# Performance work log

Hardware: AMD Instinct MI355X
Metric: run time of the kernel (lower is better)

The kernel has to match this reference:

```python
import jax, jax.numpy as jnp
import numpy as np

L, D, H, F = 4, 1024, 16, 4096  # layers, d_model, heads, ffn hidden
DH = D // H
B, S = 2, 1024


def layer_norm(x, g, b, eps=1e-12):
    m = jnp.mean(x, axis=-1, keepdims=True)
    v = jnp.mean((x - m) ** 2, axis=-1, keepdims=True)
    return (x - m) / jnp.sqrt(v + eps) * g + b


def setup_inputs() -> dict:
    key = jax.random.key(0)
    ks = jax.random.split(key, 8)
    std = 0.02
    inp = {
        'x': jax.random.normal(ks[0], (B, S, D), dtype=jnp.float32),
        'attn_mask': jnp.ones((B, S), dtype=jnp.int32),
        'Wq': jax.random.normal(ks[1], (L, D, D), dtype=jnp.float32) * std,
        'bq': jnp.zeros((L, D), dtype=jnp.float32),
        'Wk': jax.random.normal(ks[2], (L, D, D), dtype=jnp.float32) * std,
        'bk': jnp.zeros((L, D), dtype=jnp.float32),
        'Wv': jax.random.normal(ks[3], (L, D, D), dtype=jnp.float32) * std,
        'bv': jnp.zeros((L, D), dtype=jnp.float32),
        'Wo': jax.random.normal(ks[4], (L, D, D), dtype=jnp.float32) * std,
        'bo': jnp.zeros((L, D), dtype=jnp.float32),
        'ln1_g': jnp.ones((L, D), dtype=jnp.float32),
        'ln1_b': jnp.zeros((L, D), dtype=jnp.float32),
        'W1': jax.random.normal(ks[5], (L, D, F), dtype=jnp.float32) * std,
        'b1': jnp.zeros((L, F), dtype=jnp.float32),
        'W2': jax.random.normal(ks[6], (L, F, D), dtype=jnp.float32) * std,
        'b2': jnp.zeros((L, D), dtype=jnp.float32),
        'ln2_g': jnp.ones((L, D), dtype=jnp.float32),
        'ln2_b': jnp.zeros((L, D), dtype=jnp.float32),
    }
    return inp


def _block(h, mask, Wq, bq, Wk, bk, Wv, bv, Wo, bo, ln1_g, ln1_b, W1, b1, W2, b2, ln2_g, ln2_b):
    b, s, _ = h.shape
    def heads(t):
        return t.reshape(b, s, H, DH).transpose(0, 2, 1, 3)  # (b, h, s, dh)
    q = heads(jnp.einsum('bsd,de->bse', h, Wq) + bq) / jnp.sqrt(jnp.float32(DH))
    k = heads(jnp.einsum('bsd,de->bse', h, Wk) + bk)
    v = heads(jnp.einsum('bsd,de->bse', h, Wv) + bv)
    scores = jnp.einsum('bhqd,bhkd->bhqk', q, k)
    scores = jnp.where(mask[:, None, None, :] == 0, -jnp.inf, scores)
    w = jax.nn.softmax(scores, axis=-1)
    ctx = jnp.einsum('bhqk,bhkd->bhqd', w, v)
    ctx = ctx.transpose(0, 2, 1, 3).reshape(b, s, D)
    sa = jnp.einsum('bsd,de->bse', ctx, Wo) + bo
    h = layer_norm(sa + h, ln1_g, ln1_b)
    ff = jnp.einsum('bsd,df->bsf', h, W1) + b1
    ff = jax.nn.gelu(ff, approximate=False)
    ff = jnp.einsum('bsf,fd->bsd', ff, W2) + b2
    return layer_norm(ff + h, ln2_g, ln2_b)


def reference(x, attn_mask, Wq, bq, Wk, bk, Wv, bv, Wo, bo, ln1_g, ln1_b, W1, b1, W2, b2, ln2_g, ln2_b):
    h = x
    for i in range(L):
        h = _block(h, attn_mask, Wq[i], bq[i], Wk[i], bk[i], Wv[i], bv[i], Wo[i], bo[i],
                   ln1_g[i], ln1_b[i], W1[i], b1[i], W2[i], b2[i], ln2_g[i], ln2_b[i])
    return h
```

## Files before the change

kernel.cpp:

```cpp
#include <hip/hip_runtime.h>
#include <cstdint>
#include <cstddef>

using bf16x8 = __attribute__((ext_vector_type(8))) short;
using f32x4  = __attribute__((ext_vector_type(4))) float;

__device__ __forceinline__ unsigned short f2bf(float f) {
  unsigned int u = __builtin_bit_cast(unsigned int, f);
  u += 0x7fffu + ((u >> 16) & 1u);
  return (unsigned short)(u >> 16);
}
__device__ __forceinline__ float bf2f(unsigned short h) {
  unsigned int u = ((unsigned int)h) << 16;
  return __builtin_bit_cast(float, u);
}

__device__ __forceinline__ void async_cp16(const void* g, void* l) {
  __builtin_amdgcn_global_load_lds(
      (__attribute__((address_space(1))) void*)(g),
      (__attribute__((address_space(3))) void*)(l), 16, 0, 0);
}

struct EpParams {
  const float* bias;
  const float* bias2;
  const float* bias3;
  const float* res;
  float* outf;
  unsigned short* outb;
  unsigned short* outb2;
  unsigned short* outb3;
  long long strideCz;
  int ldC;
  int pair_base;
};

template <int BM, int BN, int WGM, int WGN, int FI, int FJ, int EP>
__global__ __launch_bounds__(256, 2) void gemm_bt(
    const unsigned short* __restrict__ A, const unsigned short* __restrict__ B,
    int K, int kTiles, long long strideAz, long long strideBz, EpParams p) {
  __shared__ alignas(16) unsigned short As[BM * 64];
  __shared__ alignas(16) unsigned short Bs[BN * 64];
  const int t = threadIdx.x;
  const int lane = t & 63;
  const int w = t >> 6;
  const int wr = w / WGN, wc = w % WGN;
  const int lm = lane & 15, quad = lane >> 4;
  const int m0 = blockIdx.y * BM, n0 = blockIdx.x * BN;
  const int bz = blockIdx.z;
  A += (long long)bz * strideAz;
  B += (long long)bz * strideBz;

  f32x4 acc[FI][FJ] = {};

  const int rowA = t >> 3;
  const int colSw = ((t & 7) ^ (rowA & 7)) * 8;

  for (int kt = 0; kt < kTiles; ++kt) {
    const unsigned short* ga = A + (size_t)(m0 + rowA) * K + kt * 64 + colSw;
    const unsigned short* gb = B + (size_t)(n0 + rowA) * K + kt * 64 + colSw;
#pragma unroll
    for (int s = 0; s < BM / 32; ++s)
      async_cp16(ga + (size_t)s * 32 * K, &As[s * 2048 + t * 8]);
#pragma unroll
    for (int s = 0; s < BN / 32; ++s)
      async_cp16(gb + (size_t)s * 32 * K, &Bs[s * 2048 + t * 8]);
    __syncthreads();
#pragma unroll
    for (int ks = 0; ks < 2; ++ks) {
      bf16x8 af[FI], bfr[FJ];
#pragma unroll
      for (int i = 0; i < FI; ++i) {
        int ra = wr * FI * 16 + i * 16 + lm;
        af[i] = *(const bf16x8*)&As[ra * 64 + (((ks * 4 + quad) ^ (ra & 7)) << 3)];
      }
#pragma unroll
      for (int j = 0; j < FJ; ++j) {
        int rb = wc * FJ * 16 + j * 16 + lm;
        bfr[j] = *(const bf16x8*)&Bs[rb * 64 + (((ks * 4 + quad) ^ (rb & 7)) << 3)];
      }
#pragma unroll
      for (int i = 0; i < FI; ++i)
#pragma unroll
        for (int j = 0; j < FJ; ++j)
          acc[i][j] = __builtin_amdgcn_mfma_f32_16x16x32_bf16(af[i], bfr[j], acc[i][j], 0, 0, 0);
    }
    __syncthreads();
  }

#pragma unroll
  for (int i = 0; i < FI; ++i) {
#pragma unroll
    for (int j = 0; j < FJ; ++j) {
#pragma unroll
      for (int r = 0; r < 4; ++r) {
        int row = m0 + wr * FI * 16 + i * 16 + quad * 4 + r;
        int col = n0 + wc * FJ * 16 + j * 16 + lm;
        float v = acc[i][j][r];
        if constexpr (EP == 1) {
          p.outb[(long long)bz * p.strideCz + ((size_t)row << 10) + col] = f2bf(v);
        } else if constexpr (EP == 0) {
          int bb = row >> 10, s = row & 1023;
          if (col < 1024) {
            float q = (v + p.bias[col]) * 0.125f;
            int hd = col >> 6, dh = col & 63;
            p.outb[((size_t)(bb * 16 + hd) << 16) + (s << 6) + dh] = f2bf(q);
          } else if (col < 2048) {
            int c2 = col - 1024;
            float kk = v + p.bias2[c2];
            int hd = c2 >> 6, dh = c2 & 63;
            p.outb2[((size_t)(bb * 16 + hd) << 16) + (s << 6) + dh] = f2bf(kk);
          } else {
            int c3 = col - 2048;
            float vv = v + p.bias3[c3];
            int hd = c3 >> 6, dh = c3 & 63;
            p.outb3[((size_t)(bb * 16 + hd) << 16) + ((size_t)dh << 10) + s] = f2bf(vv);
          }
        } else if constexpr (EP == 2) {
          int pair = p.pair_base + bz;
          int bb = pair >> 4, hd = pair & 15;
          p.outb[((size_t)bb << 20) + ((size_t)row << 10) + (hd << 6) + col] = f2bf(v);
        } else if constexpr (EP == 3) {
          size_t idx = (size_t)row * p.ldC + col;
          float add = (bz == 0) ? (p.bias[col] + p.res[idx]) : 0.0f;
          p.outf[(long long)bz * p.strideCz + idx] = v + add;
        } else if constexpr (EP == 4) {
          float val = v + p.bias[col];
          float g = 0.5f * val * (1.0f + erff(val * 0.70710678118654752f));
          p.outb[(size_t)row * p.ldC + col] = f2bf(g);
        }
      }
    }
  }
}

__global__ __launch_bounds__(256) void transpose_w(
    const float* __restrict__ Wq, const float* __restrict__ Wk,
    const float* __restrict__ Wv, const float* __restrict__ Wo,
    const float* __restrict__ W1, const float* __restrict__ W2,
    unsigned short* __restrict__ wqkv, unsigned short* __restrict__ wo,
    unsigned short* __restrict__ w1, unsigned short* __restrict__ w2) {
  int blk = blockIdx.x;
  int kind, local;
  if (blk < 1024) { kind = blk >> 8; local = blk & 255; }
  else if (blk < 2048) { kind = 4; local = blk - 1024; }
  else { kind = 5; local = blk - 2048; }
  const float* src;
  unsigned short* dst;
  int K, N;
  switch (kind) {
    case 0: src = Wq; dst = wqkv;                  K = 1024; N = 1024; break;
    case 1: src = Wk; dst = wqkv + 1024 * 1024;    K = 1024; N = 1024; break;
    case 2: src = Wv; dst = wqkv + 2048 * 1024;    K = 1024; N = 1024; break;
    case 3: src = Wo; dst = wo;                    K = 1024; N = 1024; break;
    case 4: src = W1; dst = w1;                    K = 1024; N = 4096; break;
    default: src = W2; dst = w2;                   K = 4096; N = 1024; break;
  }
  int tilesK = K >> 6;
  int tk = local % tilesK, tn = local / tilesK;
  int k0 = tk << 6, n0 = tn << 6;
  __shared__ float lds[64][65];
  int t = threadIdx.x;
  int rr = t >> 4, cc = (t & 15) * 4;
#pragma unroll
  for (int pp = 0; pp < 4; ++pp) {
    float4 v = *(const float4*)&src[(size_t)(k0 + rr + pp * 16) * N + n0 + cc];
    lds[rr + pp * 16][cc + 0] = v.x;
    lds[rr + pp * 16][cc + 1] = v.y;
    lds[rr + pp * 16][cc + 2] = v.z;
    lds[rr + pp * 16][cc + 3] = v.w;
  }
  __syncthreads();
#pragma unroll
  for (int pp = 0; pp < 4; ++pp) {
    int nr = rr + pp * 16;
    ushort4 o;
    o.x = f2bf(lds[cc + 0][nr]);
    o.y = f2bf(lds[cc + 1][nr]);
    o.z = f2bf(lds[cc + 2][nr]);
    o.w = f2bf(lds[cc + 3][nr]);
    *(ushort4*)&dst[(size_t)(n0 + nr) * K + k0 + cc] = o;
  }
}

__global__ __launch_bounds__(256) void cvt_bf16(const float* __restrict__ in,
                                                unsigned short* __restrict__ out) {
  int i = (blockIdx.x * 256 + threadIdx.x) * 4;
  float4 v = *(const float4*)&in[i];
  ushort4 o;
  o.x = f2bf(v.x); o.y = f2bf(v.y); o.z = f2bf(v.z); o.w = f2bf(v.w);
  *(ushort4*)&out[i] = o;
}

__global__ __launch_bounds__(256) void softmax_k(unsigned short* __restrict__ Sc,
                                                 const int* __restrict__ mask) {
  int rowid = blockIdx.x;
  int pair = rowid >> 10;
  int q = rowid & 1023;
  int bb = pair >> 4;
  unsigned short* srow = Sc + ((size_t)pair << 20) + ((size_t)q << 10);
  const int* mrow = mask + (bb << 10);
  int t = threadIdx.x;
  ushort4 s4 = *(const ushort4*)&srow[t * 4];
  int4 m4 = *(const int4*)&mrow[t * 4];
  float v0 = m4.x ? bf2f(s4.x) : -1e30f;
  float v1 = m4.y ? bf2f(s4.y) : -1e30f;
  float v2 = m4.z ? bf2f(s4.z) : -1e30f;
  float v3 = m4.w ? bf2f(s4.w) : -1e30f;
  float mx = fmaxf(fmaxf(v0, v1), fmaxf(v2, v3));
  for (int o = 32; o > 0; o >>= 1) mx = fmaxf(mx, __shfl_xor(mx, o));
  __shared__ float red[4];
  __shared__ float red2[4];
  if ((t & 63) == 0) red[t >> 6] = mx;
  __syncthreads();
  mx = fmaxf(fmaxf(red[0], red[1]), fmaxf(red[2], red[3]));
  float e0 = (v0 > -1e29f) ? __expf(v0 - mx) : 0.f;
  float e1 = (v1 > -1e29f) ? __expf(v1 - mx) : 0.f;
  float e2 = (v2 > -1e29f) ? __expf(v2 - mx) : 0.f;
  float e3 = (v3 > -1e29f) ? __expf(v3 - mx) : 0.f;
  float sum = e0 + e1 + e2 + e3;
  for (int o = 32; o > 0; o >>= 1) sum += __shfl_xor(sum, o);
  if ((t & 63) == 0) red2[t >> 6] = sum;
  __syncthreads();
  sum = red2[0] + red2[1] + red2[2] + red2[3];
  float inv = 1.0f / sum;
  ushort4 o4;
  o4.x = f2bf(e0 * inv); o4.y = f2bf(e1 * inv);
  o4.z = f2bf(e2 * inv); o4.w = f2bf(e3 * inv);
  *(ushort4*)&srow[t * 4] = o4;
}

__global__ __launch_bounds__(256) void ln_k(const float* __restrict__ in,
                                            const float* __restrict__ in2,
                                            const float* __restrict__ g,
                                            const float* __restrict__ b,
                                            float* __restrict__ outf,
                                            unsigned short* __restrict__ outb) {
  int row = blockIdx.x;
  int t = threadIdx.x;
  const float* x = in + ((size_t)row << 10);
  const float* x2 = in2 + ((size_t)row << 10);
  float4 v = *(const float4*)&x[t * 4];
  float4 v2 = *(const float4*)&x2[t * 4];
  v.x += v2.x; v.y += v2.y; v.z += v2.z; v.w += v2.w;
  float s1 = v.x + v.y + v.z + v.w;
  float s2 = v.x * v.x + v.y * v.y + v.z * v.z + v.w * v.w;
  for (int o = 32; o > 0; o >>= 1) {
    s1 += __shfl_xor(s1, o);
    s2 += __shfl_xor(s2, o);
  }
  __shared__ float r1[4], r2[4];
  if ((t & 63) == 0) { r1[t >> 6] = s1; r2[t >> 6] = s2; }
  __syncthreads();
  s1 = r1[0] + r1[1] + r1[2] + r1[3];
  s2 = r2[0] + r2[1] + r2[2] + r2[3];
  float mean = s1 * (1.0f / 1024.0f);
  float var = s2 * (1.0f / 1024.0f) - mean * mean;
  float rstd = rsqrtf(var + 1e-12f);
  float4 gg = *(const float4*)&g[t * 4];
  float4 bb = *(const float4*)&b[t * 4];
  float o0 = (v.x - mean) * rstd * gg.x + bb.x;
  float o1 = (v.y - mean) * rstd * gg.y + bb.y;
  float o2 = (v.z - mean) * rstd * gg.z + bb.z;
  float o3 = (v.w - mean) * rstd * gg.w + bb.w;
  float4 of = make_float4(o0, o1, o2, o3);
  *(float4*)&outf[((size_t)row << 10) + t * 4] = of;
  ushort4 ob;
  ob.x = f2bf(o0); ob.y = f2bf(o1); ob.z = f2bf(o2); ob.w = f2bf(o3);
  *(ushort4*)&outb[((size_t)row << 10) + t * 4] = ob;
}

extern "C" void kernel_launch(void* const* d_in, const int* in_sizes, int n_in,
                              void* d_out, int out_size, void* d_ws, size_t ws_size,
                              hipStream_t stream) {
  (void)in_sizes; (void)n_in; (void)out_size; (void)ws_size;
  const float* x    = (const float*)d_in[0];
  const int*   mask = (const int*)d_in[1];
  const float* Wq   = (const float*)d_in[2];
  const float* bq   = (const float*)d_in[3];
  const float* Wk   = (const float*)d_in[4];
  const float* bk   = (const float*)d_in[5];
  const float* Wv   = (const float*)d_in[6];
  const float* bv   = (const float*)d_in[7];
  const float* Wo   = (const float*)d_in[8];
  const float* bo   = (const float*)d_in[9];
  const float* ln1g = (const float*)d_in[10];
  const float* ln1b = (const float*)d_in[11];
  const float* W1   = (const float*)d_in[12];
  const float* b1   = (const float*)d_in[13];
  const float* W2   = (const float*)d_in[14];
  const float* b2   = (const float*)d_in[15];
  const float* ln2g = (const float*)d_in[16];
  const float* ln2b = (const float*)d_in[17];
  float* out = (float*)d_out;

  char* wsp = (char*)d_ws;
  auto take = [&](size_t bytes) { char* r = wsp; wsp += bytes; return r; };
  unsigned short* wqkv = (unsigned short*)take(3072ull * 1024 * 2);
  unsigned short* wo_t = (unsigned short*)take(1024ull * 1024 * 2);
  unsigned short* w1_t = (unsigned short*)take(4096ull * 1024 * 2);
  unsigned short* w2_t = (unsigned short*)take(1024ull * 4096 * 2);
  float*          h    = (float*)take(2048ull * 1024 * 4);
  unsigned short* hbf  = (unsigned short*)take(2048ull * 1024 * 2);
  unsigned short* Qb   = (unsigned short*)take(2048ull * 1024 * 2);
  unsigned short* Kbuf = (unsigned short*)take(2048ull * 1024 * 2);
  unsigned short* VTb  = (unsigned short*)take(2048ull * 1024 * 2);
  unsigned short* ctxb = (unsigned short*)take(2048ull * 1024 * 2);
  float*          tmp  = (float*)take(2ull * 2048 * 1024 * 4);
  unsigned short* scr  = (unsigned short*)take(32ull * 1024 * 1024 * 2);
  unsigned short* ffb  = scr;
  const long long TMPZ = 2048ll * 1024;

  cvt_bf16<<<2048, 256, 0, stream>>>(x, hbf);

  for (int l = 0; l < 4; ++l) {
    transpose_w<<<3072, 256, 0, stream>>>(
        Wq + (size_t)l * 1048576, Wk + (size_t)l * 1048576,
        Wv + (size_t)l * 1048576, Wo + (size_t)l * 1048576,
        W1 + (size_t)l * 4194304, W2 + (size_t)l * 4194304,
        wqkv, wo_t, w1_t, w2_t);

    {
      EpParams p{};
      p.bias = bq + l * 1024; p.bias2 = bk + l * 1024; p.bias3 = bv + l * 1024;
      p.outb = Qb; p.outb2 = Kbuf; p.outb3 = VTb;
      gemm_bt<64, 128, 2, 2, 2, 4, 0><<<dim3(24, 32, 1), 256, 0, stream>>>(
          hbf, wqkv, 1024, 16, 0, 0, p);
    }

    {
      EpParams p{};
      p.outb = scr; p.strideCz = 1 << 20;
      gemm_bt<128, 128, 2, 2, 4, 4, 1><<<dim3(8, 8, 32), 256, 0, stream>>>(
          Qb, Kbuf, 64, 1, 65536, 65536, p);
    }
    softmax_k<<<32768, 256, 0, stream>>>(scr, mask);
    {
      EpParams p{};
      p.outb = ctxb; p.pair_base = 0;
      gemm_bt<64, 64, 2, 2, 2, 2, 2><<<dim3(1, 16, 32), 256, 0, stream>>>(
          scr, VTb, 1024, 16, 1 << 20, 65536, p);
    }

    {
      EpParams p{};
      p.bias = bo + l * 1024; p.res = (l == 0 ? x : h);
      p.outf = tmp; p.strideCz = TMPZ; p.ldC = 1024;
      gemm_bt<128, 64, 2, 2, 4, 2, 3><<<dim3(16, 16, 2), 256, 0, stream>>>(
          ctxb, wo_t, 1024, 8, 512, 512, p);
    }
    ln_k<<<2048, 256, 0, stream>>>(tmp, tmp + TMPZ,
                                   ln1g + l * 1024, ln1b + l * 1024, h, hbf);

    {
      EpParams p{};
      p.bias = b1 + l * 4096; p.outb = ffb; p.ldC = 4096;
      gemm_bt<64, 128, 2, 2, 2, 4, 4><<<dim3(32, 32, 1), 256, 0, stream>>>(
          hbf, w1_t, 1024, 16, 0, 0, p);
    }
    {
      EpParams p{};
      p.bias = b2 + l * 1024; p.res = h;
      p.outf = tmp; p.strideCz = TMPZ; p.ldC = 1024;
      gemm_bt<128, 64, 2, 2, 4, 2, 3><<<dim3(16, 16, 2), 256, 0, stream>>>(
          ffb, w2_t, 4096, 32, 2048, 2048, p);
    }
    ln_k<<<2048, 256, 0, stream>>>(tmp, tmp + TMPZ,
                                   ln2g + l * 1024, ln2b + l * 1024,
                                   (l == 3 ? out : h), hbf);
  }
}
```

Baseline: 1.015 ms.

## Fuse QK^T, softmax and PV into a single flash-attention kernel

Replaces the three-kernel attention path (score GEMM writing a 32x1024x1024 bf16 score matrix, a separate softmax pass, then the PV GEMM) with one flash-attention kernel that uses online softmax over 128-key tiles held in LDS. This removes the large score-matrix round trips through global memory and two kernel launches per layer. In exchange the kernel launches only 512 blocks with serialized per-tile work, which may limit occupancy, and the probabilities are rounded to bf16 before PV as before.

```diff
diff --git a/kernel.cpp b/kernel.cpp
--- a/kernel.cpp
+++ b/kernel.cpp
@@ -97,9 +97,7 @@
         int row = m0 + wr * FI * 16 + i * 16 + quad * 4 + r;
         int col = n0 + wc * FJ * 16 + j * 16 + lm;
         float v = acc[i][j][r];
-        if constexpr (EP == 1) {
-          p.outb[(long long)bz * p.strideCz + ((size_t)row << 10) + col] = f2bf(v);
-        } else if constexpr (EP == 0) {
+        if constexpr (EP == 0) {
           int bb = row >> 10, s = row & 1023;
           if (col < 1024) {
             float q = (v + p.bias[col]) * 0.125f;
@@ -116,10 +114,6 @@
             int hd = c3 >> 6, dh = c3 & 63;
             p.outb3[((size_t)(bb * 16 + hd) << 16) + ((size_t)dh << 10) + s] = f2bf(vv);
           }
-        } else if constexpr (EP == 2) {
-          int pair = p.pair_base + bz;
-          int bb = pair >> 4, hd = pair & 15;
-          p.outb[((size_t)bb << 20) + ((size_t)row << 10) + (hd << 6) + col] = f2bf(v);
         } else if constexpr (EP == 3) {
           size_t idx = (size_t)row * p.ldC + col;
           float add = (bz == 0) ? (p.bias[col] + p.res[idx]) : 0.0f;
@@ -131,6 +125,162 @@
         }
       }
     }
+  }
+}
+
+__global__ __launch_bounds__(256, 2) void flash_attn(
+    const unsigned short* __restrict__ Qb, const unsigned short* __restrict__ Kb,
+    const unsigned short* __restrict__ VTb, const int* __restrict__ mask,
+    unsigned short* __restrict__ ctx) {
+  __shared__ alignas(16) unsigned short Qs[64 * 64];
+  __shared__ alignas(16) unsigned short Ks[128 * 64];
+  __shared__ alignas(16) unsigned short VTs[64 * 128];
+  __shared__ alignas(16) unsigned short Ps[64 * 128];
+  const int t = threadIdx.x;
+  const int lane = t & 63;
+  const int w = t >> 6;
+  const int lm = lane & 15, quad = lane >> 4;
+  const int pair = blockIdx.y;
+  const int q0 = blockIdx.x * 64;
+  const int bb = pair >> 4, hd = pair & 15;
+  const unsigned short* Qp = Qb + ((size_t)pair << 16);
+  const unsigned short* Kp = Kb + ((size_t)pair << 16);
+  const unsigned short* Vp = VTb + ((size_t)pair << 16);
+  const int* mrow = mask + (bb << 10);
+
+  {
+    const int rowA = t >> 3;
+    const int c = t & 7;
+#pragma unroll
+    for (int s = 0; s < 2; ++s) {
+      int row = s * 32 + rowA;
+      async_cp16(Qp + (size_t)(q0 + row) * 64 + ((c ^ (row & 7)) << 3),
+                 &Qs[s * 2048 + t * 8]);
+    }
+  }
+
+  f32x4 o_acc[4] = {};
+  float m_run[4], l_run[4];
+#pragma unroll
+  for (int r = 0; r < 4; ++r) { m_run[r] = -3e38f; l_run[r] = 0.f; }
+
+  for (int k0 = 0; k0 < 1024; k0 += 128) {
+    __syncthreads();
+    {
+      const int rowA = t >> 3;
+      const int c = t & 7;
+#pragma unroll
+      for (int s = 0; s < 4; ++s) {
+        int row = s * 32 + rowA;
+        async_cp16(Kp + (size_t)(k0 + row) * 64 + ((c ^ (row & 7)) << 3),
+                   &Ks[s * 2048 + t * 8]);
+      }
+      const int rowV = t >> 4;
+      const int cv = t & 15;
+#pragma unroll
+      for (int s = 0; s < 4; ++s) {
+        int row = s * 16 + rowV;
+        async_cp16(Vp + (size_t)row * 1024 + k0 + ((cv ^ (row & 15)) << 3),
+                   &VTs[s * 2048 + t * 8]);
+      }
+    }
+    int mv[8];
+#pragma unroll
+    for (int j = 0; j < 8; ++j) mv[j] = mrow[k0 + j * 16 + lm];
+    __syncthreads();
+
+    f32x4 s_acc[8] = {};
+    {
+      const int ra = w * 16 + lm;
+      bf16x8 aq[2];
+#pragma unroll
+      for (int ks = 0; ks < 2; ++ks)
+        aq[ks] = *(const bf16x8*)&Qs[ra * 64 + (((ks * 4 + quad) ^ (ra & 7)) << 3)];
+#pragma unroll
+      for (int j = 0; j < 8; ++j) {
+        const int rb = j * 16 + lm;
+#pragma unroll
+        for (int ks = 0; ks < 2; ++ks) {
+          bf16x8 bk_ = *(const bf16x8*)&Ks[rb * 64 + (((ks * 4 + quad) ^ (rb & 7)) << 3)];
+          s_acc[j] = __builtin_amdgcn_mfma_f32_16x16x32_bf16(aq[ks], bk_, s_acc[j], 0, 0, 0);
+        }
+      }
+    }
+
+    float mt[4];
+#pragma unroll
+    for (int r = 0; r < 4; ++r) mt[r] = -3e38f;
+#pragma unroll
+    for (int j = 0; j < 8; ++j)
+#pragma unroll
+      for (int r = 0; r < 4; ++r) {
+        float sv = mv[j] ? s_acc[j][r] : -1e30f;
+        s_acc[j][r] = sv;
+        mt[r] = fmaxf(mt[r], sv);
+      }
+#pragma unroll
+    for (int r = 0; r < 4; ++r)
+#pragma unroll
+      for (int off = 1; off < 16; off <<= 1)
+        mt[r] = fmaxf(mt[r], __shfl_xor(mt[r], off));
+    float alpha[4], lt[4];
+#pragma unroll
+    for (int r = 0; r < 4; ++r) {
+      float mn = fmaxf(m_run[r], mt[r]);
+      alpha[r] = __expf(m_run[r] - mn);
+      m_run[r] = mn;
+      lt[r] = 0.f;
+    }
+#pragma unroll
+    for (int j = 0; j < 8; ++j)
+#pragma unroll
+      for (int r = 0; r < 4; ++r) {
+        float pv = __expf(s_acc[j][r] - m_run[r]);
+        s_acc[j][r] = pv;
+        lt[r] += pv;
+      }
+#pragma unroll
+    for (int r = 0; r < 4; ++r) {
+#pragma unroll
+      for (int off = 1; off < 16; off <<= 1) lt[r] += __shfl_xor(lt[r], off);
+      l_run[r] = l_run[r] * alpha[r] + lt[r];
+    }
+#pragma unroll
+    for (int jf = 0; jf < 4; ++jf)
+#pragma unroll
+      for (int r = 0; r < 4; ++r) o_acc[jf][r] *= alpha[r];
+
+#pragma unroll
+    for (int j = 0; j < 8; ++j) {
+      const int chunk = 2 * j + (lm >> 3);
+#pragma unroll
+      for (int r = 0; r < 4; ++r) {
+        const int row = w * 16 + quad * 4 + r;
+        Ps[row * 128 + ((chunk ^ (row & 15)) << 3) + (lm & 7)] = f2bf(s_acc[j][r]);
+      }
+    }
+
+    const int ra = w * 16 + lm;
+#pragma unroll
+    for (int kk = 0; kk < 4; ++kk) {
+      bf16x8 ap = *(const bf16x8*)&Ps[ra * 128 + (((kk * 4 + quad) ^ (ra & 15)) << 3)];
+#pragma unroll
+      for (int jf = 0; jf < 4; ++jf) {
+        const int rb = jf * 16 + lm;
+        bf16x8 bv_ = *(const bf16x8*)&VTs[rb * 128 + (((kk * 4 + quad) ^ (rb & 15)) << 3)];
+        o_acc[jf] = __builtin_amdgcn_mfma_f32_16x16x32_bf16(ap, bv_, o_acc[jf], 0, 0, 0);
+      }
+    }
+  }
+
+#pragma unroll
+  for (int r = 0; r < 4; ++r) {
+    float inv = 1.0f / l_run[r];
+    int row = q0 + w * 16 + quad * 4 + r;
+#pragma unroll
+    for (int jf = 0; jf < 4; ++jf)
+      ctx[((size_t)bb << 20) + ((size_t)row << 10) + (hd << 6) + jf * 16 + lm] =
+          f2bf(o_acc[jf][r] * inv);
   }
 }
 
@@ -190,44 +340,6 @@
   ushort4 o;
   o.x = f2bf(v.x); o.y = f2bf(v.y); o.z = f2bf(v.z); o.w = f2bf(v.w);
   *(ushort4*)&out[i] = o;
-}
-
-__global__ __launch_bounds__(256) void softmax_k(unsigned short* __restrict__ Sc,
-                                                 const int* __restrict__ mask) {
-  int rowid = blockIdx.x;
-  int pair = rowid >> 10;
-  int q = rowid & 1023;
-  int bb = pair >> 4;
-  unsigned short* srow = Sc + ((size_t)pair << 20) + ((size_t)q << 10);
-  const int* mrow = mask + (bb << 10);
-  int t = threadIdx.x;
-  ushort4 s4 = *(const ushort4*)&srow[t * 4];
-  int4 m4 = *(const int4*)&mrow[t * 4];
-  float v0 = m4.x ? bf2f(s4.x) : -1e30f;
-  float v1 = m4.y ? bf2f(s4.y) : -1e30f;
-  float v2 = m4.z ? bf2f(s4.z) : -1e30f;
-  float v3 = m4.w ? bf2f(s4.w) : -1e30f;
-  float mx = fmaxf(fmaxf(v0, v1), fmaxf(v2, v3));
-  for (int o = 32; o > 0; o >>= 1) mx = fmaxf(mx, __shfl_xor(mx, o));
-  __shared__ float red[4];
-  __shared__ float red2[4];
-  if ((t & 63) == 0) red[t >> 6] = mx;
-  __syncthreads();
-  mx = fmaxf(fmaxf(red[0], red[1]), fmaxf(red[2], red[3]));
-  float e0 = (v0 > -1e29f) ? __expf(v0 - mx) : 0.f;
-  float e1 = (v1 > -1e29f) ? __expf(v1 - mx) : 0.f;
-  float e2 = (v2 > -1e29f) ? __expf(v2 - mx) : 0.f;
-  float e3 = (v3 > -1e29f) ? __expf(v3 - mx) : 0.f;
-  float sum = e0 + e1 + e2 + e3;
-  for (int o = 32; o > 0; o >>= 1) sum += __shfl_xor(sum, o);
-  if ((t & 63) == 0) red2[t >> 6] = sum;
-  __syncthreads();
-  sum = red2[0] + red2[1] + red2[2] + red2[3];
-  float inv = 1.0f / sum;
-  ushort4 o4;
-  o4.x = f2bf(e0 * inv); o4.y = f2bf(e1 * inv);
-  o4.z = f2bf(e2 * inv); o4.w = f2bf(e3 * inv);
-  *(ushort4*)&srow[t * 4] = o4;
 }
 
 __global__ __launch_bounds__(256) void ln_k(const float* __restrict__ in,
@@ -307,8 +419,7 @@
   unsigned short* VTb  = (unsigned short*)take(2048ull * 1024 * 2);
   unsigned short* ctxb = (unsigned short*)take(2048ull * 1024 * 2);
   float*          tmp  = (float*)take(2ull * 2048 * 1024 * 4);
-  unsigned short* scr  = (unsigned short*)take(32ull * 1024 * 1024 * 2);
-  unsigned short* ffb  = scr;
+  unsigned short* ffb  = (unsigned short*)take(2048ull * 4096 * 2);
   const long long TMPZ = 2048ll * 1024;
 
   cvt_bf16<<<2048, 256, 0, stream>>>(x, hbf);
@@ -328,19 +439,7 @@
           hbf, wqkv, 1024, 16, 0, 0, p);
     }
 
-    {
-      EpParams p{};
-      p.outb = scr; p.strideCz = 1 << 20;
-      gemm_bt<128, 128, 2, 2, 4, 4, 1><<<dim3(8, 8, 32), 256, 0, stream>>>(
-          Qb, Kbuf, 64, 1, 65536, 65536, p);
-    }
-    softmax_k<<<32768, 256, 0, stream>>>(scr, mask);
-    {
-      EpParams p{};
-      p.outb = ctxb; p.pair_base = 0;
-      gemm_bt<64, 64, 2, 2, 2, 2, 2><<<dim3(1, 16, 32), 256, 0, stream>>>(
-          scr, VTb, 1024, 16, 1 << 20, 65536, p);
-    }
+    flash_attn<<<dim3(16, 32), 256, 0, stream>>>(Qb, Kbuf, VTb, mask, ctxb);
 
     {
       EpParams p{};
```

Result: faster. 824.4 us (-18.7%).
